# Optimization experiments

Measured on AMD Instinct MI355X. Metric: run time of the kernel, lower is better.

Reference implementation:

```python
import jax, jax.numpy as jnp
import numpy as np

IMG_W, IMG_H = 1024.0, 681.0
N_PROPOSALS = 256
N_TARGETS = 32
NUM_PRED_CLASSES = 51
FG_THRESH = 0.5
BG_THRESH = 0.3
BELOW_LOW_THRESHOLD = -1
BETWEEN_THRESHOLDS = -2
TO_REMOVE = 1.0


def _make_boxes(key, n, w, h):
    kxy, kwh = jax.random.split(key)
    xy = jax.random.uniform(kxy, (n, 2)) * jnp.array([w * 0.7, h * 0.7])
    wh = jax.random.uniform(kwh, (n, 2)) * jnp.array([w * 0.3, h * 0.3]) + 8.0
    return jnp.concatenate([xy, xy + wh], axis=1).astype(jnp.float32)  # xyxy


def setup_inputs() -> dict:
    key = jax.random.key(0)
    k1, k2, k3 = jax.random.split(key, 3)
    proposal_boxes = _make_boxes(k1, N_PROPOSALS, IMG_W, IMG_H)
    target_boxes = _make_boxes(k2, N_TARGETS, IMG_W, IMG_H)
    # pred_labels field has one predicate label per ordered GT pair (M*M)
    target_pair_labels = jax.random.randint(
        k3, (N_TARGETS * N_TARGETS,), 0, NUM_PRED_CLASSES, dtype=jnp.int64)
    return {
        'proposal_boxes': proposal_boxes,
        'target_boxes': target_boxes,
        'target_pair_labels': target_pair_labels,
    }


def _boxlist_iou(a, b):
    # a: [M,4], b: [N,4] in xyxy -> IoU [M,N] with the +1 pixel convention
    area_a = (a[:, 2] - a[:, 0] + TO_REMOVE) * (a[:, 3] - a[:, 1] + TO_REMOVE)
    area_b = (b[:, 2] - b[:, 0] + TO_REMOVE) * (b[:, 3] - b[:, 1] + TO_REMOVE)
    lt = jnp.maximum(a[:, None, :2], b[None, :, :2])  # [M,N,2]
    rb = jnp.minimum(a[:, None, 2:], b[None, :, 2:])  # [M,N,2]
    wh = jnp.clip(rb - lt + TO_REMOVE, 0.0)
    inter = wh[..., 0] * wh[..., 1]
    return inter / (area_a[:, None] + area_b[None, :] - inter)


def reference(proposal_boxes, target_boxes, target_pair_labels):
    N = proposal_boxes.shape[0]
    M = target_boxes.shape[0]
    # static off-diagonal index set over the N*N ordered proposal pairs
    offdiag = np.nonzero(~np.eye(N, dtype=bool).ravel())[0]  # [N*(N-1)]

    # --- pairwise match quality: ((iou_i + iou_j)/2) for every GT pair ---
    iou = _boxlist_iou(target_boxes, proposal_boxes)  # [M,N]
    quality = 0.5 * (iou[:, None, :, None] + iou[None, :, None, :])  # [M,M,N,N]
    quality = quality.reshape(M * M, N * N)[:, offdiag]  # [M*M, N*(N-1)]

    # --- GT box pairs [M*M, 8] ---
    tb_subj = jnp.broadcast_to(target_boxes[:, None, :], (M, M, 4))
    tb_obj = jnp.broadcast_to(target_boxes[None, :, :], (M, M, 4))
    target_box_pairs = jnp.concatenate([tb_subj, tb_obj], axis=-1).reshape(M * M, 8)

    # --- proposal box/idx pairs with self-pairs removed ---
    pb_subj = jnp.broadcast_to(proposal_boxes[:, None, :], (N, N, 4))
    pb_obj = jnp.broadcast_to(proposal_boxes[None, :, :], (N, N, 4))
    proposal_box_pairs = jnp.concatenate([pb_subj, pb_obj], axis=-1)
    proposal_box_pairs = proposal_box_pairs.reshape(N * N, 8)[offdiag]
    ii, jj = jnp.meshgrid(jnp.arange(N), jnp.arange(N), indexing='ij')
    proposal_idx_pairs = jnp.stack([ii.reshape(-1), jj.reshape(-1)], axis=1)[offdiag]

    # --- Matcher: best GT pair per proposal pair, with fg/bg thresholds ---
    matched_vals = jnp.max(quality, axis=0)      # [N*(N-1)]
    matches = jnp.argmax(quality, axis=0)        # [N*(N-1)]
    matched_idxs = jnp.where(matched_vals < BG_THRESH, BELOW_LOW_THRESHOLD, matches)
    matched_idxs = jnp.where(
        (matched_vals >= BG_THRESH) & (matched_vals < FG_THRESH),
        BETWEEN_THRESHOLDS, matched_idxs)

    # --- labels: gather GT-pair labels at clamped matches, mark bg/ignore ---
    labels = target_pair_labels[jnp.clip(matched_idxs, 0)].astype(jnp.int64)
    labels = jnp.where(matched_idxs == BELOW_LOW_THRESHOLD, 0, labels)
    labels = jnp.where(matched_idxs == BETWEEN_THRESHOLDS, -1, labels)

    return (quality, matched_idxs, labels, proposal_box_pairs,
            proposal_idx_pairs, target_box_pairs)
```

## Files before the change

### kernel.cpp

```cpp
#include <hip/hip_runtime.h>

#define N_P 256
#define N_T 32
#define OFFDIAG 65280
#define QROWS 1024

__global__ void iou_best_kernel(const float* __restrict__ pb,
                                const float* __restrict__ tb,
                                float* __restrict__ iou,
                                float* __restrict__ bv,
                                int* __restrict__ bidx) {
    __shared__ float t0[N_T], t1[N_T], t2[N_T], t3[N_T], ta[N_T];
    int tid = threadIdx.x;
    if (tid < N_T) {
        float a0 = tb[tid * 4 + 0], a1 = tb[tid * 4 + 1];
        float a2 = tb[tid * 4 + 2], a3 = tb[tid * 4 + 3];
        t0[tid] = a0; t1[tid] = a1; t2[tid] = a2; t3[tid] = a3;
        ta[tid] = ((a2 - a0) + 1.0f) * ((a3 - a1) + 1.0f);
    }
    __syncthreads();
    int p = tid;
    float b0 = pb[p * 4 + 0], b1 = pb[p * 4 + 1];
    float b2 = pb[p * 4 + 2], b3 = pb[p * 4 + 3];
    float areaB = ((b2 - b0) + 1.0f) * ((b3 - b1) + 1.0f);
    float bestv = -1.0f;
    int besti = 0;
    #pragma unroll
    for (int t = 0; t < N_T; ++t) {
        float lt0 = fmaxf(t0[t], b0), lt1 = fmaxf(t1[t], b1);
        float rb0 = fminf(t2[t], b2), rb1 = fminf(t3[t], b3);
        float w = fmaxf((rb0 - lt0) + 1.0f, 0.0f);
        float h = fmaxf((rb1 - lt1) + 1.0f, 0.0f);
        float inter = w * h;
        float v = inter / ((ta[t] + areaB) - inter);
        iou[t * N_P + p] = v;
        if (v > bestv) { bestv = v; besti = t; }
    }
    bv[p] = bestv;
    bidx[p] = besti;
}

__global__ void quality_kernel(const float* __restrict__ iou,
                               float* __restrict__ qout) {
    int pq = blockIdx.y;
    int p = pq >> 5, q = pq & 31;
    __shared__ float rp[N_P], rq[N_P];
    int tid = threadIdx.x;
    rp[tid] = iou[p * N_P + tid];
    rq[tid] = iou[q * N_P + tid];
    __syncthreads();
    int base = blockIdx.x * 1024 + tid * 4;
    if (base < OFFDIAG) {
        float4 v;
        float* vv = reinterpret_cast<float*>(&v);
        #pragma unroll
        for (int e = 0; e < 4; ++e) {
            int k = base + e;
            int i = (unsigned)k / 255u;
            int r = k - i * 255;
            int j = r + (r >= i ? 1 : 0);
            vv[e] = 0.5f * (rp[i] + rq[j]);
        }
        *reinterpret_cast<float4*>(qout + (size_t)pq * OFFDIAG + base) = v;
    }
}

__global__ void tail_kernel(const float* __restrict__ pb,
                            const float* __restrict__ tb,
                            const int* __restrict__ tpl,
                            const float* __restrict__ bv,
                            const int* __restrict__ bidx,
                            float* __restrict__ out) {
    int k = blockIdx.x * 256 + threadIdx.x;
    float* matched = out + (size_t)QROWS * OFFDIAG;
    float* labels  = matched + OFFDIAG;
    float* pbp     = labels + OFFDIAG;
    float* pip     = pbp + (size_t)OFFDIAG * 8;
    float* tbp     = pip + (size_t)OFFDIAG * 2;

    int i = (unsigned)k / 255u;
    int r = k - i * 255;
    int j = r + (r >= i ? 1 : 0);

    float mv = 0.5f * (bv[i] + bv[j]);
    int mi, lab;
    if (mv < 0.3f)      { mi = -1; lab = 0; }
    else if (mv < 0.5f) { mi = -2; lab = -1; }
    else                { mi = bidx[i] * N_T + bidx[j]; lab = tpl[mi]; }

    matched[k] = (float)mi;
    labels[k]  = (float)lab;

    float4 bi = reinterpret_cast<const float4*>(pb)[i];
    float4 bj = reinterpret_cast<const float4*>(pb)[j];
    reinterpret_cast<float4*>(pbp)[k * 2 + 0] = bi;
    reinterpret_cast<float4*>(pbp)[k * 2 + 1] = bj;
    pip[k * 2 + 0] = (float)i;
    pip[k * 2 + 1] = (float)j;

    if (k < QROWS) {
        int p = k >> 5, q = k & 31;
        reinterpret_cast<float4*>(tbp)[k * 2 + 0] =
            reinterpret_cast<const float4*>(tb)[p];
        reinterpret_cast<float4*>(tbp)[k * 2 + 1] =
            reinterpret_cast<const float4*>(tb)[q];
    }
}

extern "C" void kernel_launch(void* const* d_in, const int* in_sizes, int n_in,
                              void* d_out, int out_size, void* d_ws, size_t ws_size,
                              hipStream_t stream) {
    const float* pb  = (const float*)d_in[0];
    const float* tb  = (const float*)d_in[1];
    const int*   tpl = (const int*)d_in[2];
    float* out = (float*)d_out;

    float* iou  = (float*)d_ws;
    float* bv   = iou + N_T * N_P;
    int*   bidx = (int*)(bv + N_P);

    iou_best_kernel<<<1, 256, 0, stream>>>(pb, tb, iou, bv, bidx);
    quality_kernel<<<dim3(64, QROWS), 256, 0, stream>>>(iou, out);
    tail_kernel<<<OFFDIAG / 256, 256, 0, stream>>>(pb, tb, tpl, bv, bidx, out);
}
```

Before: 56.22 us.

## Fuse IoU, quality and tail kernels into one launch with recomputed IoU

```diff
diff --git a/kernel.cpp b/kernel.cpp
--- a/kernel.cpp
+++ b/kernel.cpp
@@ -4,106 +4,114 @@
 #define N_T 32
 #define OFFDIAG 65280
 #define QROWS 1024
+#define QBLOCKS (QROWS * 64)
+#define TAILBLKS 255
 
-__global__ void iou_best_kernel(const float* __restrict__ pb,
-                                const float* __restrict__ tb,
-                                float* __restrict__ iou,
-                                float* __restrict__ bv,
-                                int* __restrict__ bidx) {
-    __shared__ float t0[N_T], t1[N_T], t2[N_T], t3[N_T], ta[N_T];
-    int tid = threadIdx.x;
-    if (tid < N_T) {
-        float a0 = tb[tid * 4 + 0], a1 = tb[tid * 4 + 1];
-        float a2 = tb[tid * 4 + 2], a3 = tb[tid * 4 + 3];
-        t0[tid] = a0; t1[tid] = a1; t2[tid] = a2; t3[tid] = a3;
-        ta[tid] = ((a2 - a0) + 1.0f) * ((a3 - a1) + 1.0f);
-    }
-    __syncthreads();
-    int p = tid;
-    float b0 = pb[p * 4 + 0], b1 = pb[p * 4 + 1];
-    float b2 = pb[p * 4 + 2], b3 = pb[p * 4 + 3];
-    float areaB = ((b2 - b0) + 1.0f) * ((b3 - b1) + 1.0f);
-    float bestv = -1.0f;
-    int besti = 0;
-    #pragma unroll
-    for (int t = 0; t < N_T; ++t) {
-        float lt0 = fmaxf(t0[t], b0), lt1 = fmaxf(t1[t], b1);
-        float rb0 = fminf(t2[t], b2), rb1 = fminf(t3[t], b3);
-        float w = fmaxf((rb0 - lt0) + 1.0f, 0.0f);
-        float h = fmaxf((rb1 - lt1) + 1.0f, 0.0f);
-        float inter = w * h;
-        float v = inter / ((ta[t] + areaB) - inter);
-        iou[t * N_P + p] = v;
-        if (v > bestv) { bestv = v; besti = t; }
-    }
-    bv[p] = bestv;
-    bidx[p] = besti;
+__device__ __forceinline__ float iou_one(float a0, float a1, float a2, float a3,
+                                         float ta,
+                                         float b0, float b1, float b2, float b3,
+                                         float areaB) {
+    float lt0 = fmaxf(a0, b0), lt1 = fmaxf(a1, b1);
+    float rb0 = fminf(a2, b2), rb1 = fminf(a3, b3);
+    float w = fmaxf((rb0 - lt0) + 1.0f, 0.0f);
+    float h = fmaxf((rb1 - lt1) + 1.0f, 0.0f);
+    float inter = w * h;
+    return inter / ((ta + areaB) - inter);
 }
 
-__global__ void quality_kernel(const float* __restrict__ iou,
-                               float* __restrict__ qout) {
-    int pq = blockIdx.y;
-    int p = pq >> 5, q = pq & 31;
-    __shared__ float rp[N_P], rq[N_P];
+__global__ void relpn_fused_kernel(const float* __restrict__ pb,
+                                   const float* __restrict__ tb,
+                                   const int* __restrict__ tpl,
+                                   float* __restrict__ out) {
     int tid = threadIdx.x;
-    rp[tid] = iou[p * N_P + tid];
-    rq[tid] = iou[q * N_P + tid];
-    __syncthreads();
-    int base = blockIdx.x * 1024 + tid * 4;
-    if (base < OFFDIAG) {
-        float4 v;
-        float* vv = reinterpret_cast<float*>(&v);
-        #pragma unroll
-        for (int e = 0; e < 4; ++e) {
-            int k = base + e;
+    unsigned blk = blockIdx.x;
+
+    if (blk < QBLOCKS) {
+        unsigned pq = blk >> 6;
+        unsigned seg = blk & 63u;
+        int p = pq >> 5, q = pq & 31;
+
+        __shared__ float rp[N_P], rq[N_P];
+        float pa0 = tb[p * 4 + 0], pa1 = tb[p * 4 + 1];
+        float pa2 = tb[p * 4 + 2], pa3 = tb[p * 4 + 3];
+        float pta = ((pa2 - pa0) + 1.0f) * ((pa3 - pa1) + 1.0f);
+        float qa0 = tb[q * 4 + 0], qa1 = tb[q * 4 + 1];
+        float qa2 = tb[q * 4 + 2], qa3 = tb[q * 4 + 3];
+        float qta = ((qa2 - qa0) + 1.0f) * ((qa3 - qa1) + 1.0f);
+
+        float4 B = reinterpret_cast<const float4*>(pb)[tid];
+        float areaB = ((B.z - B.x) + 1.0f) * ((B.w - B.y) + 1.0f);
+        rp[tid] = 0.5f * iou_one(pa0, pa1, pa2, pa3, pta, B.x, B.y, B.z, B.w, areaB);
+        rq[tid] = 0.5f * iou_one(qa0, qa1, qa2, qa3, qta, B.x, B.y, B.z, B.w, areaB);
+        __syncthreads();
+
+        int f = (int)seg * 256 + tid;
+        if (f * 4 < OFFDIAG) {
+            int k = f * 4;
             int i = (unsigned)k / 255u;
             int r = k - i * 255;
-            int j = r + (r >= i ? 1 : 0);
-            vv[e] = 0.5f * (rp[i] + rq[j]);
+            float4 v;
+            float* vv = reinterpret_cast<float*>(&v);
+            #pragma unroll
+            for (int e = 0; e < 4; ++e) {
+                if (r >= 255) { r -= 255; ++i; }
+                int j = r + (r >= i ? 1 : 0);
+                vv[e] = rp[i] + rq[j];
+                ++r;
+            }
+            reinterpret_cast<float4*>(out + (size_t)pq * OFFDIAG)[f] = v;
         }
-        *reinterpret_cast<float4*>(qout + (size_t)pq * OFFDIAG + base) = v;
-    }
-}
+    } else {
+        int k = (int)(blk - QBLOCKS) * 256 + tid;
+        float* matched = out + (size_t)QROWS * OFFDIAG;
+        float* labels  = matched + OFFDIAG;
+        float* pbp     = labels + OFFDIAG;
+        float* pip     = pbp + (size_t)OFFDIAG * 8;
+        float* tbp     = pip + (size_t)OFFDIAG * 2;
 
-__global__ void tail_kernel(const float* __restrict__ pb,
-                            const float* __restrict__ tb,
-                            const int* __restrict__ tpl,
-                            const float* __restrict__ bv,
-                            const int* __restrict__ bidx,
-                            float* __restrict__ out) {
-    int k = blockIdx.x * 256 + threadIdx.x;
-    float* matched = out + (size_t)QROWS * OFFDIAG;
-    float* labels  = matched + OFFDIAG;
-    float* pbp     = labels + OFFDIAG;
-    float* pip     = pbp + (size_t)OFFDIAG * 8;
-    float* tbp     = pip + (size_t)OFFDIAG * 2;
+        int i = (unsigned)k / 255u;
+        int r = k - i * 255;
+        int j = r + (r >= i ? 1 : 0);
 
-    int i = (unsigned)k / 255u;
-    int r = k - i * 255;
-    int j = r + (r >= i ? 1 : 0);
+        float4 Bi = reinterpret_cast<const float4*>(pb)[i];
+        float4 Bj = reinterpret_cast<const float4*>(pb)[j];
+        float areaBi = ((Bi.z - Bi.x) + 1.0f) * ((Bi.w - Bi.y) + 1.0f);
+        float areaBj = ((Bj.z - Bj.x) + 1.0f) * ((Bj.w - Bj.y) + 1.0f);
 
-    float mv = 0.5f * (bv[i] + bv[j]);
-    int mi, lab;
-    if (mv < 0.3f)      { mi = -1; lab = 0; }
-    else if (mv < 0.5f) { mi = -2; lab = -1; }
-    else                { mi = bidx[i] * N_T + bidx[j]; lab = tpl[mi]; }
+        float bvi = -1.0f, bvj = -1.0f;
+        int bii = 0, bij = 0;
+        #pragma unroll
+        for (int t = 0; t < N_T; ++t) {
+            float a0 = tb[t * 4 + 0], a1 = tb[t * 4 + 1];
+            float a2 = tb[t * 4 + 2], a3 = tb[t * 4 + 3];
+            float ta = ((a2 - a0) + 1.0f) * ((a3 - a1) + 1.0f);
+            float vi = iou_one(a0, a1, a2, a3, ta, Bi.x, Bi.y, Bi.z, Bi.w, areaBi);
+            float vj = iou_one(a0, a1, a2, a3, ta, Bj.x, Bj.y, Bj.z, Bj.w, areaBj);
+            if (vi > bvi) { bvi = vi; bii = t; }
+            if (vj > bvj) { bvj = vj; bij = t; }
+        }
 
-    matched[k] = (float)mi;
-    labels[k]  = (float)lab;
+        float mv = 0.5f * (bvi + bvj);
+        int mi, lab;
+        if (mv < 0.3f)      { mi = -1; lab = 0; }
+        else if (mv < 0.5f) { mi = -2; lab = -1; }
+        else                { mi = bii * N_T + bij; lab = tpl[mi]; }
 
-    float4 bi = reinterpret_cast<const float4*>(pb)[i];
-    float4 bj = reinterpret_cast<const float4*>(pb)[j];
-    reinterpret_cast<float4*>(pbp)[k * 2 + 0] = bi;
-    reinterpret_cast<float4*>(pbp)[k * 2 + 1] = bj;
-    pip[k * 2 + 0] = (float)i;
-    pip[k * 2 + 1] = (float)j;
+        matched[k] = (float)mi;
+        labels[k]  = (float)lab;
 
-    if (k < QROWS) {
-        int p = k >> 5, q = k & 31;
-        reinterpret_cast<float4*>(tbp)[k * 2 + 0] =
-            reinterpret_cast<const float4*>(tb)[p];
-        reinterpret_cast<float4*>(tbp)[k * 2 + 1] =
-            reinterpret_cast<const float4*>(tb)[q];
+        reinterpret_cast<float4*>(pbp)[k * 2 + 0] = Bi;
+        reinterpret_cast<float4*>(pbp)[k * 2 + 1] = Bj;
+        pip[k * 2 + 0] = (float)i;
+        pip[k * 2 + 1] = (float)j;
+
+        if (k < QROWS) {
+            int pp = k >> 5, qq = k & 31;
+            reinterpret_cast<float4*>(tbp)[k * 2 + 0] =
+                reinterpret_cast<const float4*>(tb)[pp];
+            reinterpret_cast<float4*>(tbp)[k * 2 + 1] =
+                reinterpret_cast<const float4*>(tb)[qq];
+        }
     }
 }
 
@@ -115,11 +123,5 @@
     const int*   tpl = (const int*)d_in[2];
     float* out = (float*)d_out;
 
-    float* iou  = (float*)d_ws;
-    float* bv   = iou + N_T * N_P;
-    int*   bidx = (int*)(bv + N_P);
-
-    iou_best_kernel<<<1, 256, 0, stream>>>(pb, tb, iou, bv, bidx);
-    quality_kernel<<<dim3(64, QROWS), 256, 0, stream>>>(iou, out);
-    tail_kernel<<<OFFDIAG / 256, 256, 0, stream>>>(pb, tb, tpl, bv, bidx, out);
+    relpn_fused_kernel<<<QBLOCKS + TAILBLKS, 256, 0, stream>>>(pb, tb, tpl, out);
 }
```

Result: slower. 86.78 us (+54.4%).

## Restructure quality kernel to one block per GT pair with row-wise scalar stores

Applied to the files above, without the earlier changes.

```diff
diff --git a/kernel.cpp b/kernel.cpp
--- a/kernel.cpp
+++ b/kernel.cpp
@@ -42,26 +42,29 @@
 
 __global__ void quality_kernel(const float* __restrict__ iou,
                                float* __restrict__ qout) {
-    int pq = blockIdx.y;
+    int pq = blockIdx.x;
     int p = pq >> 5, q = pq & 31;
     __shared__ float rp[N_P], rq[N_P];
     int tid = threadIdx.x;
-    rp[tid] = iou[p * N_P + tid];
-    rq[tid] = iou[q * N_P + tid];
+    rp[tid] = 0.5f * iou[p * N_P + tid];
+    rq[tid] = 0.5f * iou[q * N_P + tid];
     __syncthreads();
-    int base = blockIdx.x * 1024 + tid * 4;
-    if (base < OFFDIAG) {
-        float4 v;
-        float* vv = reinterpret_cast<float*>(&v);
+
+    int wave = tid >> 6, lane = tid & 63;
+    float* dst = qout + (size_t)pq * OFFDIAG;
+
+    for (int i0 = wave; i0 < N_P; i0 += 4) {
+        int i = __builtin_amdgcn_readfirstlane(i0);
+        float a = rp[i];
+        int ibase = i * 255;
         #pragma unroll
-        for (int e = 0; e < 4; ++e) {
-            int k = base + e;
-            int i = (unsigned)k / 255u;
-            int r = k - i * 255;
-            int j = r + (r >= i ? 1 : 0);
-            vv[e] = 0.5f * (rp[i] + rq[j]);
+        for (int m = 0; m < 4; ++m) {
+            int pos = m * 64 + lane;
+            if (pos < 255) {
+                int j = pos + (pos >= i ? 1 : 0);
+                dst[ibase + pos] = a + rq[j];
+            }
         }
-        *reinterpret_cast<float4*>(qout + (size_t)pq * OFFDIAG + base) = v;
     }
 }
 
@@ -99,11 +102,11 @@
     pip[k * 2 + 1] = (float)j;
 
     if (k < QROWS) {
-        int p = k >> 5, q = k & 31;
+        int pp = k >> 5, qq = k & 31;
         reinterpret_cast<float4*>(tbp)[k * 2 + 0] =
-            reinterpret_cast<const float4*>(tb)[p];
+            reinterpret_cast<const float4*>(tb)[pp];
         reinterpret_cast<float4*>(tbp)[k * 2 + 1] =
-            reinterpret_cast<const float4*>(tb)[q];
+            reinterpret_cast<const float4*>(tb)[qq];
     }
 }
 
@@ -120,6 +123,6 @@
     int*   bidx = (int*)(bv + N_P);
 
     iou_best_kernel<<<1, 256, 0, stream>>>(pb, tb, iou, bv, bidx);
-    quality_kernel<<<dim3(64, QROWS), 256, 0, stream>>>(iou, out);
+    quality_kernel<<<QROWS, 256, 0, stream>>>(iou, out);
     tail_kernel<<<OFFDIAG / 256, 256, 0, stream>>>(pb, tb, tpl, bv, bidx, out);
 }
```

Result: faster. 52.90 us (-5.9%).
